# Kernel optimization log

Measured on AMD Instinct MI355X. Metric: run time of the kernel, lower is better.

## Reference

```python
import jax, jax.numpy as jnp
import numpy as np

K = 27          # kernel_size^3
N_IN = 150000   # active input sites
N_OUT = 150000  # active output sites
C_IN = 64
C_OUT = 64
R = 50000       # rules per kernel offset (equal counts -> vectorized grouped GEMM)


def setup_inputs() -> dict:
    key = jax.random.key(0)
    k1, k2, k3, k4 = jax.random.split(key, 4)
    # kaiming_normal_ fan_out, relu: std = sqrt(2 / fan_out) with fan_out = C_OUT
    w_std = float(np.sqrt(2.0 / C_OUT))
    return {
        "x_data": jax.random.normal(k1, (N_IN, C_IN), dtype=jnp.float32),
        "weights": jax.random.normal(k2, (K, C_IN, C_OUT), dtype=jnp.float32) * w_std,
        "bias": jnp.zeros((C_OUT,), dtype=jnp.float32),
        "in_idx": jax.random.randint(k3, (K * R,), 0, N_IN, dtype=jnp.int32),
        "out_idx": jax.random.randint(k4, (K * R,), 0, N_OUT, dtype=jnp.int32),
    }


def reference(x_data, weights, bias, in_idx, out_idx):
    # Rulebook sparse 3D conv: per-offset gather -> GEMM -> scatter-add.
    gathered = x_data[in_idx].reshape(K, R, C_IN)           # [K, R, Cin]
    vals = jnp.einsum('krc,kco->kro', gathered, weights)    # [K, R, Cout]
    out = jnp.zeros((N_OUT, C_OUT), dtype=x_data.dtype)
    out = out.at[out_idx].add(vals.reshape(K * R, C_OUT))   # atomic scatter-add
    return out + bias[None, :]
```

## Files before the change

kernel.cpp:

```cpp
#include <hip/hip_runtime.h>
#include <hip/hip_bf16.h>


typedef __bf16 bf16x8_t __attribute__((ext_vector_type(8)));
typedef __bf16 bf16x2_t __attribute__((ext_vector_type(2)));
typedef float f32x4_t __attribute__((ext_vector_type(4)));

#define KOFF 27
#define RULES 50000
#define KR (KOFF * RULES)
#define CIN 64
#define COUT 64
#define NIN 150000
#define NOUT 150000

#define BR1 128
#define BPK1 ((RULES + BR1 - 1) / BR1)
#define BRF 256
#define BPKF ((RULES + BRF - 1) / BRF)

#define NB1 ((NOUT + 1023) / 1024)

#define OFF_OFF 0ull
#define OFF_BSUM 600064ull
#define OFF_BSCAN 600832ull
#define OFF_RANK 601600ull
#define OFF_XB 6001664ull
#define OFF_VALS 25201664ull
#define WS_FULL (25201664ull + 172800000ull)

__device__ __forceinline__ void gload_lds16(const void* g, void* l) {
  __builtin_amdgcn_global_load_lds(
      (const __attribute__((address_space(1))) unsigned int*)g,
      (__attribute__((address_space(3))) unsigned int*)l, 16, 0, 0);
}

__global__ __launch_bounds__(256) void k_cvt_zero(const float* __restrict__ x,
                                                  __bf16* __restrict__ xb,
                                                  int* __restrict__ cnt) {
  const int i = blockIdx.x * 256 + threadIdx.x;
  if (i < NIN * CIN / 8) {
    const float4 f0 = reinterpret_cast<const float4*>(x)[i * 2];
    const float4 f1 = reinterpret_cast<const float4*>(x)[i * 2 + 1];
    bf16x8_t v;
    v[0] = (__bf16)f0.x; v[1] = (__bf16)f0.y; v[2] = (__bf16)f0.z; v[3] = (__bf16)f0.w;
    v[4] = (__bf16)f1.x; v[5] = (__bf16)f1.y; v[6] = (__bf16)f1.z; v[7] = (__bf16)f1.w;
    reinterpret_cast<bf16x8_t*>(xb)[i] = v;
  }
  if (i <= NOUT) cnt[i] = 0;
}

__global__ __launch_bounds__(256) void k_count(const int* __restrict__ out_idx,
                                               int* __restrict__ cnt,
                                               int* __restrict__ rankl) {
  const int i = blockIdx.x * 256 + threadIdx.x;
  if (i < KR / 4) {
    const int4 v = reinterpret_cast<const int4*>(out_idx)[i];
    int4 r;
    r.x = atomicAdd(&cnt[v.x], 1);
    r.y = atomicAdd(&cnt[v.y], 1);
    r.z = atomicAdd(&cnt[v.z], 1);
    r.w = atomicAdd(&cnt[v.w], 1);
    reinterpret_cast<int4*>(rankl)[i] = r;
  }
}

__global__ __launch_bounds__(1024) void k_scan1(int* __restrict__ off,
                                                int* __restrict__ bsum) {
  __shared__ int s[1024];
  const int t = threadIdx.x;
  const int i = blockIdx.x * 1024 + t;
  const int v = (i < NOUT) ? off[i] : 0;
  s[t] = v;
  __syncthreads();
#pragma unroll
  for (int d = 1; d < 1024; d <<= 1) {
    const int u = (t >= d) ? s[t - d] : 0;
    __syncthreads();
    s[t] += u;
    __syncthreads();
  }
  if (i < NOUT) off[i] = s[t] - v;
  if (t == 1023) bsum[blockIdx.x] = s[1023];
}

__global__ __launch_bounds__(256) void k_scan2(const int* __restrict__ bsum,
                                               int* __restrict__ bscan, int nb) {
  __shared__ int s[256];
  const int t = threadIdx.x;
  const int v = (t < nb) ? bsum[t] : 0;
  s[t] = v;
  __syncthreads();
#pragma unroll
  for (int d = 1; d < 256; d <<= 1) {
    const int u = (t >= d) ? s[t - d] : 0;
    __syncthreads();
    s[t] += u;
    __syncthreads();
  }
  if (t < nb) bscan[t] = s[t] - v;
}

__global__ __launch_bounds__(256) void pass1_bf16(
    const __bf16* __restrict__ xb, const float* __restrict__ w,
    const int* __restrict__ in_idx, const int* __restrict__ out_idx,
    const int* __restrict__ off_arr, const int* __restrict__ bscan,
    const int* __restrict__ rankl, __bf16* __restrict__ vals) {
  __shared__ char lds[BR1 * 128 + 64 * 128];
  __shared__ int lds_dst[BR1];
  char* const Abase = lds;
  char* const Bbase = lds + BR1 * 128;

  const int bid = blockIdx.x;
  const int k = bid / BPK1;
  const int rblk = bid - k * BPK1;
  const int rule0 = rblk * BR1;
  const int t = threadIdx.x;
  const int wid = t >> 6;
  const int lane = t & 63;

  {
    const int rowInWave = lane >> 3;
    const int srcChunk = (lane & 7) ^ rowInWave;
    const int* idxBase = in_idx + (size_t)k * RULES;
#pragma unroll
    for (int it = 0; it < 4; ++it) {
      const int rbase = it * 32 + wid * 8;
      int rule = rule0 + rbase + rowInWave;
      if (rule > RULES - 1) rule = RULES - 1;
      const int src = idxBase[rule];
      const __bf16* gp = xb + ((size_t)src << 6) + (srcChunk << 3);
      gload_lds16(gp, Abase + rbase * 128 + lane * 16);
    }
  }

  if (t < BR1) {
    const int rule = rule0 + t;
    if (rule < RULES) {
      const size_t gi = (size_t)k * RULES + rule;
      const int orow = out_idx[gi];
      lds_dst[t] = off_arr[orow] + bscan[orow >> 10] + rankl[gi];
    }
  }

  {
    const int c = t >> 2;
    const int o0 = (t & 3) * 16;
    const float* wp = w + ((size_t)k * CIN + c) * COUT + o0;
#pragma unroll
    for (int j4 = 0; j4 < 4; ++j4) {
      const float4 f = *reinterpret_cast<const float4*>(wp + j4 * 4);
#pragma unroll
      for (int e = 0; e < 4; ++e) {
        const int o = o0 + j4 * 4 + e;
        const float val = (e == 0) ? f.x : (e == 1) ? f.y : (e == 2) ? f.z : f.w;
        const int addr = o * 128 + ((c * 2) ^ ((o & 7) << 4));
        *reinterpret_cast<__bf16*>(Bbase + addr) = (__bf16)val;
      }
    }
  }

  __syncthreads();

  const int rA = lane & 15;
  const int g = lane >> 4;

  bf16x8_t af[2][2];
  bf16x8_t bfr[4][2];
#pragma unroll
  for (int m = 0; m < 2; ++m)
#pragma unroll
    for (int kk = 0; kk < 2; ++kk) {
      const int r = wid * 32 + m * 16 + rA;
      const int colByte = (kk * 64 + g * 16) ^ ((r & 7) << 4);
      af[m][kk] = *reinterpret_cast<const bf16x8_t*>(Abase + r * 128 + colByte);
    }
#pragma unroll
  for (int n = 0; n < 4; ++n)
#pragma unroll
    for (int kk = 0; kk < 2; ++kk) {
      const int o = n * 16 + rA;
      const int colByte = (kk * 64 + g * 16) ^ ((o & 7) << 4);
      bfr[n][kk] = *reinterpret_cast<const bf16x8_t*>(Bbase + o * 128 + colByte);
    }

  __syncthreads();

  f32x4_t acc[2][4];
#pragma unroll
  for (int m = 0; m < 2; ++m)
#pragma unroll
    for (int n = 0; n < 4; ++n)
#pragma unroll
      for (int e = 0; e < 4; ++e) acc[m][n][e] = 0.0f;

#pragma unroll
  for (int kk = 0; kk < 2; ++kk)
#pragma unroll
    for (int m = 0; m < 2; ++m)
#pragma unroll
      for (int n = 0; n < 4; ++n)
        acc[m][n] = __builtin_amdgcn_mfma_f32_16x16x32_bf16(
            af[m][kk], bfr[n][kk], acc[m][n], 0, 0, 0);

  const bool evenLane = (rA & 1) == 0;
#pragma unroll
  for (int m = 0; m < 2; ++m) {
#pragma unroll
    for (int j = 0; j < 4; ++j) {
      const int rr = wid * 32 + m * 16 + g * 4 + j;
      float mine[4], other[4];
#pragma unroll
      for (int n = 0; n < 4; ++n) {
        mine[n] = acc[m][n][j];
        other[n] = __shfl_xor(mine[n], 1, 64);
      }
      const int swz = (rr & 7) << 4;
      if (evenLane) {
#pragma unroll
        for (int n = 0; n < 2; ++n) {
          bf16x2_t p; p[0] = (__bf16)mine[n]; p[1] = (__bf16)other[n];
          const int col = n * 16 + rA;
          *reinterpret_cast<bf16x2_t*>(Abase + rr * 128 + ((col * 2) ^ swz)) = p;
        }
      } else {
#pragma unroll
        for (int n = 2; n < 4; ++n) {
          bf16x2_t p; p[0] = (__bf16)other[n]; p[1] = (__bf16)mine[n];
          const int col = n * 16 + rA - 1;
          *reinterpret_cast<bf16x2_t*>(Abase + rr * 128 + ((col * 2) ^ swz)) = p;
        }
      }
    }
  }

  __syncthreads();

  {
    const int chunk = t & 7;
    const int r0 = t >> 3;
#pragma unroll
    for (int pass = 0; pass < 4; ++pass) {
      const int r = r0 + pass * 32;
      const int rule = rule0 + r;
      if (rule < RULES) {
        const int dst = lds_dst[r];
        const bf16x8_t v = *reinterpret_cast<const bf16x8_t*>(
            Abase + r * 128 + ((chunk * 16) ^ ((r & 7) << 4)));
        *reinterpret_cast<bf16x8_t*>(vals + (size_t)dst * COUT + chunk * 8) = v;
      }
    }
  }
}

__global__ __launch_bounds__(256) void pass2_kernel(
    const __bf16* __restrict__ vals, const int* __restrict__ off,
    const int* __restrict__ bscan, const float* __restrict__ bias,
    float* __restrict__ out) {
  const int t = threadIdx.x;
  const int rloc = t >> 3;
  const int l8 = t & 7;
  const int row = blockIdx.x * 32 + rloc;
  if (row >= NOUT) return;

  const int s = off[row] + bscan[row >> 10];
  const int e = (row + 1 < NOUT) ? off[row + 1] + bscan[(row + 1) >> 10] : KR;

  const float4 b0 = reinterpret_cast<const float4*>(bias)[l8 * 2];
  const float4 b1 = reinterpret_cast<const float4*>(bias)[l8 * 2 + 1];
  float a0 = b0.x, a1 = b0.y, a2 = b0.z, a3 = b0.w;
  float a4 = b1.x, a5 = b1.y, a6 = b1.z, a7 = b1.w;

  const __bf16* vp = vals + (size_t)s * COUT + l8 * 8;
  for (int j = s; j < e; ++j, vp += COUT) {
    const bf16x8_t v = *reinterpret_cast<const bf16x8_t*>(vp);
    a0 += (float)v[0]; a1 += (float)v[1]; a2 += (float)v[2]; a3 += (float)v[3];
    a4 += (float)v[4]; a5 += (float)v[5]; a6 += (float)v[6]; a7 += (float)v[7];
  }
  float* op = out + (size_t)row * COUT + l8 * 8;
  reinterpret_cast<float4*>(op)[0] = make_float4(a0, a1, a2, a3);
  reinterpret_cast<float4*>(op)[1] = make_float4(a4, a5, a6, a7);
}

__global__ __launch_bounds__(256) void init_out_kernel(
    const float* __restrict__ bias, float* __restrict__ out, int total4) {
  const int i = blockIdx.x * blockDim.x + threadIdx.x;
  if (i < total4) {
    const float4 v = reinterpret_cast<const float4*>(bias)[i & 15];
    reinterpret_cast<float4*>(out)[i] = v;
  }
}

__global__ __launch_bounds__(256) void spconv_atomic_kernel(
    const float* __restrict__ x, const float* __restrict__ w,
    const int* __restrict__ in_idx, const int* __restrict__ out_idx,
    float* __restrict__ out) {
  __shared__ char lds[256 * 128 + 64 * 128];
  char* const Abase = lds;
  char* const Bbase = lds + 256 * 128;

  const int bid = blockIdx.x;
  const int k = bid / BPKF;
  const int rblk = bid - k * BPKF;
  const int rule0 = rblk * BRF;
  const int t = threadIdx.x;

  {
    const int chunk = t & 7;
    const int r0 = t >> 3;
#pragma unroll
    for (int pass = 0; pass < 8; ++pass) {
      const int r = r0 + pass * 32;
      const int rule = rule0 + r;
      bf16x8_t v;
      if (rule < RULES) {
        const int src = in_idx[(size_t)k * RULES + rule];
        const float* p = x + (size_t)src * CIN + chunk * 8;
        const float4 f0 = *reinterpret_cast<const float4*>(p);
        const float4 f1 = *reinterpret_cast<const float4*>(p + 4);
        v[0] = (__bf16)f0.x; v[1] = (__bf16)f0.y;
        v[2] = (__bf16)f0.z; v[3] = (__bf16)f0.w;
        v[4] = (__bf16)f1.x; v[5] = (__bf16)f1.y;
        v[6] = (__bf16)f1.z; v[7] = (__bf16)f1.w;
      } else {
#pragma unroll
        for (int e = 0; e < 8; ++e) v[e] = (__bf16)0.0f;
      }
      const int colByte = (chunk * 16) ^ ((r & 7) << 4);
      *reinterpret_cast<bf16x8_t*>(Abase + r * 128 + colByte) = v;
    }
  }
  {
    const int c = t >> 2;
    const int o0 = (t & 3) * 16;
    const float* wp = w + ((size_t)k * CIN + c) * COUT + o0;
#pragma unroll
    for (int j4 = 0; j4 < 4; ++j4) {
      const float4 f = *reinterpret_cast<const float4*>(wp + j4 * 4);
#pragma unroll
      for (int e = 0; e < 4; ++e) {
        const int o = o0 + j4 * 4 + e;
        const float val = (e == 0) ? f.x : (e == 1) ? f.y : (e == 2) ? f.z : f.w;
        const int addr = o * 128 + ((c * 2) ^ ((o & 7) << 4));
        *reinterpret_cast<__bf16*>(Bbase + addr) = (__bf16)val;
      }
    }
  }
  __syncthreads();

  const int wid = t >> 6;
  const int l = t & 63;
  const int rA = l & 15;
  const int g = l >> 4;

  bf16x8_t af[4][2];
  bf16x8_t bfr[4][2];
#pragma unroll
  for (int m = 0; m < 4; ++m)
#pragma unroll
    for (int kk = 0; kk < 2; ++kk) {
      const int r = wid * 64 + m * 16 + rA;
      const int colByte = (kk * 64 + g * 16) ^ ((r & 7) << 4);
      af[m][kk] = *reinterpret_cast<const bf16x8_t*>(Abase + r * 128 + colByte);
    }
#pragma unroll
  for (int n = 0; n < 4; ++n)
#pragma unroll
    for (int kk = 0; kk < 2; ++kk) {
      const int o = n * 16 + rA;
      const int colByte = (kk * 64 + g * 16) ^ ((o & 7) << 4);
      bfr[n][kk] = *reinterpret_cast<const bf16x8_t*>(Bbase + o * 128 + colByte);
    }

  f32x4_t acc[4][4];
#pragma unroll
  for (int m = 0; m < 4; ++m)
#pragma unroll
    for (int n = 0; n < 4; ++n)
#pragma unroll
      for (int e = 0; e < 4; ++e) acc[m][n][e] = 0.0f;

#pragma unroll
  for (int kk = 0; kk < 2; ++kk)
#pragma unroll
    for (int m = 0; m < 4; ++m)
#pragma unroll
      for (int n = 0; n < 4; ++n)
        acc[m][n] = __builtin_amdgcn_mfma_f32_16x16x32_bf16(
            af[m][kk], bfr[n][kk], acc[m][n], 0, 0, 0);

#pragma unroll
  for (int m = 0; m < 4; ++m)
#pragma unroll
    for (int j = 0; j < 4; ++j) {
      const int rr = wid * 64 + m * 16 + g * 4 + j;
      const int rule = rule0 + rr;
      if (rule < RULES) {
        const int orow = out_idx[(size_t)k * RULES + rule];
        float* op = out + (size_t)orow * COUT + rA;
#pragma unroll
        for (int n = 0; n < 4; ++n) atomicAdd(op + n * 16, acc[m][n][j]);
      }
    }
}

extern "C" void kernel_launch(void* const* d_in, const int* in_sizes, int n_in,
                              void* d_out, int out_size, void* d_ws, size_t ws_size,
                              hipStream_t stream) {
  const float* x = (const float*)d_in[0];
  const float* w = (const float*)d_in[1];
  const float* bias = (const float*)d_in[2];
  const int* in_idx = (const int*)d_in[3];
  const int* out_idx = (const int*)d_in[4];
  float* out = (float*)d_out;

  if (ws_size >= WS_FULL) {
    char* ws = (char*)d_ws;
    int* off = (int*)(ws + OFF_OFF);
    int* bsum = (int*)(ws + OFF_BSUM);
    int* bscan = (int*)(ws + OFF_BSCAN);
    int* rankl = (int*)(ws + OFF_RANK);
    __bf16* xb = (__bf16*)(ws + OFF_XB);
    __bf16* vals = (__bf16*)(ws + OFF_VALS);

    k_cvt_zero<<<(NIN * CIN / 8 + 255) / 256, 256, 0, stream>>>(x, xb, off);
    k_count<<<(KR / 4 + 255) / 256, 256, 0, stream>>>(out_idx, off, rankl);
    k_scan1<<<NB1, 1024, 0, stream>>>(off, bsum);
    k_scan2<<<1, 256, 0, stream>>>(bsum, bscan, NB1);
    pass1_bf16<<<KOFF * BPK1, 256, 0, stream>>>(xb, w, in_idx, out_idx, off,
                                                bscan, rankl, vals);
    pass2_kernel<<<(NOUT + 31) / 32, 256, 0, stream>>>(vals, off, bscan, bias,
                                                       out);
  } else {
    const int total4 = NOUT * COUT / 4;
    init_out_kernel<<<(total4 + 255) / 256, 256, 0, stream>>>(bias, out, total4);
    spconv_atomic_kernel<<<KOFF * BPKF, 256, 0, stream>>>(x, w, in_idx, out_idx, out);
  }
}
```

Baseline: 265.6 us.

## Replace stored per-rule ranks with atomic cursors; widen pass2 reduction; nontemporal accesses

The per-rule rank array written by the count kernel is removed. pass1 now claims its destination slot with an atomic increment on a per-output cursor that the scan kernel initializes, which saves the rank writes and reads. pass2 now gives each output row a full wave: four row-groups of 16 lanes each read 8-byte chunks and are combined with cross-lane shuffles, which raises parallelism for rows with many entries. Nontemporal loads and stores are added for the streamed data. The trade-off is a second round of atomics in pass1 and a nondeterministic ordering of vals within a row, which changes float summation order.

```diff
diff --git a/kernel.cpp b/kernel.cpp
--- a/kernel.cpp
+++ b/kernel.cpp
@@ -5,6 +5,8 @@
 typedef __bf16 bf16x8_t __attribute__((ext_vector_type(8)));
 typedef __bf16 bf16x2_t __attribute__((ext_vector_type(2)));
 typedef float f32x4_t __attribute__((ext_vector_type(4)));
+typedef int i32x4_t __attribute__((ext_vector_type(4)));
+typedef short s16x4_t __attribute__((ext_vector_type(4)));
 
 #define KOFF 27
 #define RULES 50000
@@ -24,15 +26,19 @@
 #define OFF_OFF 0ull
 #define OFF_BSUM 600064ull
 #define OFF_BSCAN 600832ull
-#define OFF_RANK 601600ull
-#define OFF_XB 6001664ull
-#define OFF_VALS 25201664ull
-#define WS_FULL (25201664ull + 172800000ull)
+#define OFF_CUR 601600ull
+#define OFF_XB 1201664ull
+#define OFF_VALS 20401920ull
+#define WS_FULL (20401920ull + 172800000ull)
 
 __device__ __forceinline__ void gload_lds16(const void* g, void* l) {
   __builtin_amdgcn_global_load_lds(
       (const __attribute__((address_space(1))) unsigned int*)g,
       (__attribute__((address_space(3))) unsigned int*)l, 16, 0, 0);
+}
+
+__device__ __forceinline__ float bf16bits_to_f32(short b) {
+  return __uint_as_float(((unsigned)(unsigned short)b) << 16);
 }
 
 __global__ __launch_bounds__(256) void k_cvt_zero(const float* __restrict__ x,
@@ -40,32 +46,32 @@
                                                   int* __restrict__ cnt) {
   const int i = blockIdx.x * 256 + threadIdx.x;
   if (i < NIN * CIN / 8) {
-    const float4 f0 = reinterpret_cast<const float4*>(x)[i * 2];
-    const float4 f1 = reinterpret_cast<const float4*>(x)[i * 2 + 1];
+    const f32x4_t f0 =
+        __builtin_nontemporal_load(reinterpret_cast<const f32x4_t*>(x) + i * 2);
+    const f32x4_t f1 = __builtin_nontemporal_load(
+        reinterpret_cast<const f32x4_t*>(x) + i * 2 + 1);
     bf16x8_t v;
-    v[0] = (__bf16)f0.x; v[1] = (__bf16)f0.y; v[2] = (__bf16)f0.z; v[3] = (__bf16)f0.w;
-    v[4] = (__bf16)f1.x; v[5] = (__bf16)f1.y; v[6] = (__bf16)f1.z; v[7] = (__bf16)f1.w;
+    v[0] = (__bf16)f0[0]; v[1] = (__bf16)f0[1]; v[2] = (__bf16)f0[2]; v[3] = (__bf16)f0[3];
+    v[4] = (__bf16)f1[0]; v[5] = (__bf16)f1[1]; v[6] = (__bf16)f1[2]; v[7] = (__bf16)f1[3];
     reinterpret_cast<bf16x8_t*>(xb)[i] = v;
   }
   if (i <= NOUT) cnt[i] = 0;
 }
 
 __global__ __launch_bounds__(256) void k_count(const int* __restrict__ out_idx,
-                                               int* __restrict__ cnt,
-                                               int* __restrict__ rankl) {
+                                               int* __restrict__ cnt) {
   const int i = blockIdx.x * 256 + threadIdx.x;
   if (i < KR / 4) {
     const int4 v = reinterpret_cast<const int4*>(out_idx)[i];
-    int4 r;
-    r.x = atomicAdd(&cnt[v.x], 1);
-    r.y = atomicAdd(&cnt[v.y], 1);
-    r.z = atomicAdd(&cnt[v.z], 1);
-    r.w = atomicAdd(&cnt[v.w], 1);
-    reinterpret_cast<int4*>(rankl)[i] = r;
+    atomicAdd(&cnt[v.x], 1);
+    atomicAdd(&cnt[v.y], 1);
+    atomicAdd(&cnt[v.z], 1);
+    atomicAdd(&cnt[v.w], 1);
   }
 }
 
 __global__ __launch_bounds__(1024) void k_scan1(int* __restrict__ off,
+                                                int* __restrict__ cursor,
                                                 int* __restrict__ bsum) {
   __shared__ int s[1024];
   const int t = threadIdx.x;
@@ -80,7 +86,11 @@
     s[t] += u;
     __syncthreads();
   }
-  if (i < NOUT) off[i] = s[t] - v;
+  if (i < NOUT) {
+    const int ex = s[t] - v;
+    off[i] = ex;
+    cursor[i] = ex;
+  }
   if (t == 1023) bsum[blockIdx.x] = s[1023];
 }
 
@@ -104,8 +114,8 @@
 __global__ __launch_bounds__(256) void pass1_bf16(
     const __bf16* __restrict__ xb, const float* __restrict__ w,
     const int* __restrict__ in_idx, const int* __restrict__ out_idx,
-    const int* __restrict__ off_arr, const int* __restrict__ bscan,
-    const int* __restrict__ rankl, __bf16* __restrict__ vals) {
+    int* __restrict__ cursor, const int* __restrict__ bscan,
+    __bf16* __restrict__ vals) {
   __shared__ char lds[BR1 * 128 + 64 * 128];
   __shared__ int lds_dst[BR1];
   char* const Abase = lds;
@@ -139,7 +149,8 @@
     if (rule < RULES) {
       const size_t gi = (size_t)k * RULES + rule;
       const int orow = out_idx[gi];
-      lds_dst[t] = off_arr[orow] + bscan[orow >> 10] + rankl[gi];
+      const int local = atomicAdd(&cursor[orow], 1);
+      lds_dst[t] = bscan[orow >> 10] + local;
     }
   }
 
@@ -245,9 +256,10 @@
       const int rule = rule0 + r;
       if (rule < RULES) {
         const int dst = lds_dst[r];
-        const bf16x8_t v = *reinterpret_cast<const bf16x8_t*>(
+        const i32x4_t v = *reinterpret_cast<const i32x4_t*>(
             Abase + r * 128 + ((chunk * 16) ^ ((r & 7) << 4)));
-        *reinterpret_cast<bf16x8_t*>(vals + (size_t)dst * COUT + chunk * 8) = v;
+        __builtin_nontemporal_store(
+            v, reinterpret_cast<i32x4_t*>(vals + (size_t)dst * COUT + chunk * 8));
       }
     }
   }
@@ -258,28 +270,38 @@
     const int* __restrict__ bscan, const float* __restrict__ bias,
     float* __restrict__ out) {
   const int t = threadIdx.x;
-  const int rloc = t >> 3;
-  const int l8 = t & 7;
-  const int row = blockIdx.x * 32 + rloc;
-  if (row >= NOUT) return;
+  const int row = blockIdx.x * 4 + (t >> 6);
+  const int lane = t & 63;
+  const int rp = lane >> 4;
+  const int cs = lane & 15;
 
   const int s = off[row] + bscan[row >> 10];
   const int e = (row + 1 < NOUT) ? off[row + 1] + bscan[(row + 1) >> 10] : KR;
 
-  const float4 b0 = reinterpret_cast<const float4*>(bias)[l8 * 2];
-  const float4 b1 = reinterpret_cast<const float4*>(bias)[l8 * 2 + 1];
-  float a0 = b0.x, a1 = b0.y, a2 = b0.z, a3 = b0.w;
-  float a4 = b1.x, a5 = b1.y, a6 = b1.z, a7 = b1.w;
-
-  const __bf16* vp = vals + (size_t)s * COUT + l8 * 8;
-  for (int j = s; j < e; ++j, vp += COUT) {
-    const bf16x8_t v = *reinterpret_cast<const bf16x8_t*>(vp);
-    a0 += (float)v[0]; a1 += (float)v[1]; a2 += (float)v[2]; a3 += (float)v[3];
-    a4 += (float)v[4]; a5 += (float)v[5]; a6 += (float)v[6]; a7 += (float)v[7];
-  }
-  float* op = out + (size_t)row * COUT + l8 * 8;
-  reinterpret_cast<float4*>(op)[0] = make_float4(a0, a1, a2, a3);
-  reinterpret_cast<float4*>(op)[1] = make_float4(a4, a5, a6, a7);
+  float a0 = 0.0f, a1 = 0.0f, a2 = 0.0f, a3 = 0.0f;
+  const short* vp =
+      reinterpret_cast<const short*>(vals) + (size_t)(s + rp) * COUT + cs * 4;
+  for (int j = s + rp; j < e; j += 4, vp += 4 * COUT) {
+    const s16x4_t v =
+        __builtin_nontemporal_load(reinterpret_cast<const s16x4_t*>(vp));
+    a0 += bf16bits_to_f32(v[0]);
+    a1 += bf16bits_to_f32(v[1]);
+    a2 += bf16bits_to_f32(v[2]);
+    a3 += bf16bits_to_f32(v[3]);
+  }
+
+  a0 += __shfl_xor(a0, 16, 64); a1 += __shfl_xor(a1, 16, 64);
+  a2 += __shfl_xor(a2, 16, 64); a3 += __shfl_xor(a3, 16, 64);
+  a0 += __shfl_xor(a0, 32, 64); a1 += __shfl_xor(a1, 32, 64);
+  a2 += __shfl_xor(a2, 32, 64); a3 += __shfl_xor(a3, 32, 64);
+
+  if (rp == 0) {
+    const f32x4_t b = reinterpret_cast<const f32x4_t*>(bias)[cs];
+    f32x4_t o;
+    o[0] = a0 + b[0]; o[1] = a1 + b[1]; o[2] = a2 + b[2]; o[3] = a3 + b[3];
+    __builtin_nontemporal_store(
+        o, reinterpret_cast<f32x4_t*>(out + (size_t)row * COUT + cs * 4));
+  }
 }
 
 __global__ __launch_bounds__(256) void init_out_kernel(
@@ -419,18 +441,17 @@
     int* off = (int*)(ws + OFF_OFF);
     int* bsum = (int*)(ws + OFF_BSUM);
     int* bscan = (int*)(ws + OFF_BSCAN);
-    int* rankl = (int*)(ws + OFF_RANK);
+    int* cursor = (int*)(ws + OFF_CUR);
     __bf16* xb = (__bf16*)(ws + OFF_XB);
     __bf16* vals = (__bf16*)(ws + OFF_VALS);
 
     k_cvt_zero<<<(NIN * CIN / 8 + 255) / 256, 256, 0, stream>>>(x, xb, off);
-    k_count<<<(KR / 4 + 255) / 256, 256, 0, stream>>>(out_idx, off, rankl);
-    k_scan1<<<NB1, 1024, 0, stream>>>(off, bsum);
+    k_count<<<(KR / 4 + 255) / 256, 256, 0, stream>>>(out_idx, off);
+    k_scan1<<<NB1, 1024, 0, stream>>>(off, cursor, bsum);
     k_scan2<<<1, 256, 0, stream>>>(bsum, bscan, NB1);
-    pass1_bf16<<<KOFF * BPK1, 256, 0, stream>>>(xb, w, in_idx, out_idx, off,
-                                                bscan, rankl, vals);
-    pass2_kernel<<<(NOUT + 31) / 32, 256, 0, stream>>>(vals, off, bscan, bias,
-                                                       out);
+    pass1_bf16<<<KOFF * BPK1, 256, 0, stream>>>(xb, w, in_idx, out_idx, cursor,
+                                                bscan, vals);
+    pass2_kernel<<<NOUT / 4, 256, 0, stream>>>(vals, off, bscan, bias, out);
   } else {
     const int total4 = NOUT * COUT / 4;
     init_out_kernel<<<(total4 + 255) / 256, 256, 0, stream>>>(bias, out, total4);
```

After: 294.9 us. 11.0% more time.
